# Optimization experiments

Measured on AMD Instinct MI355X. Metric: run time of the kernel, lower is better.

The kernel has to match this reference:

```python
import jax, jax.numpy as jnp
import numpy as np

KSIZE = 11
SIGMA = 1.5
CHANNELS = 1


def _gaussian_kernel(size=KSIZE, sigma=SIGMA, channels=CHANNELS):
    coords = jnp.arange(size, dtype=jnp.float32) - size // 2
    g = jnp.exp(-coords ** 2 / (2.0 * sigma ** 2))
    g = g / g.sum()
    k2d = jnp.outer(g, g)  # [k, k]
    # depthwise kernel, OIHW with I=1 per group
    return jnp.broadcast_to(k2d, (channels, 1, size, size))


def _dwconv(x, k):
    pad = KSIZE // 2
    return jax.lax.conv_general_dilated(
        x, k, window_strides=(1, 1), padding=[(pad, pad), (pad, pad)],
        dimension_numbers=('NCHW', 'OIHW', 'NCHW'),
        feature_group_count=CHANNELS)


def setup_inputs() -> dict:
    key = jax.random.key(0)
    k1, k2 = jax.random.split(key)
    x_hat = jax.random.normal(k1, (64, 1, 512, 512), dtype=jnp.float32)
    x = jax.random.normal(k2, (64, 1, 512, 512), dtype=jnp.float32)
    kernel = _gaussian_kernel()
    return {"x_hat": x_hat, "x": x, "kernel": kernel}


def reference(x_hat, x, kernel):
    C1, C2 = 0.01 ** 2, 0.03 ** 2
    # shift [-1,1] -> [0,1]
    a = (x + 1.0) / 2.0          # 'x' in _ssim
    b = (x_hat + 1.0) / 2.0      # 'y' in _ssim
    mu_x = _dwconv(a, kernel)
    mu_y = _dwconv(b, kernel)
    mu_x2 = mu_x ** 2
    mu_y2 = mu_y ** 2
    mu_xy = mu_x * mu_y
    sig_x = _dwconv(a * a, kernel) - mu_x2
    sig_y = _dwconv(b * b, kernel) - mu_y2
    sig_xy = _dwconv(a * b, kernel) - mu_xy
    num = (2.0 * mu_xy + C1) * (2.0 * sig_xy + C2)
    den = (mu_x2 + mu_y2 + C1) * (sig_x + sig_y + C2)
    ssim = (num / (den + 1e-08)).mean()
    return 1.0 - ssim
```

## Files before the change

### kernel.cpp

```cpp
#include <hip/hip_runtime.h>

#define IMG_W 512
#define IMG_H 512
#define RH    64
#define KS    11
#define KR    5
#define OFF   8
#define LROW  (OFF + IMG_W + OFF)

__global__ __launch_bounds__(256, 2)
void ssim_main(const float* __restrict__ xhat,
               const float* __restrict__ x,
               const float* __restrict__ kern,
               float* __restrict__ accum)
{
    __shared__ float rowA[LROW];
    __shared__ float rowB[LROW];
    __shared__ float red[4];

    const int tid   = threadIdx.x;
    const int c0    = tid << 1;
    const int img   = blockIdx.x >> 3;
    const int strip = blockIdx.x & 7;
    const int R0    = strip * RH;
    const float* xp = x    + (size_t)img * (IMG_W * IMG_H);
    const float* hp = xhat + (size_t)img * (IMG_W * IMG_H);

    float g[KS];
    {
        const float inv = rsqrtf(kern[5 * KS + 5]);
        #pragma unroll
        for (int i = 0; i < KS; ++i) g[i] = kern[5 * KS + i] * inv;
    }

    if (tid < OFF) {
        rowA[tid] = 0.f;                rowB[tid] = 0.f;
        rowA[OFF + IMG_W + tid] = 0.f;  rowB[OFF + IMG_W + tid] = 0.f;
    }

    float hist[5][KS][2];
    float acc = 0.f;
    const float C1 = 1e-4f, C2 = 9e-4f;

    #pragma unroll 1
    for (int rblk = 0; rblk < 77; rblk += 11) {
        #pragma unroll
        for (int p = 0; p < KS; ++p) {
            const int rr = rblk + p;
            const bool active = (rr < RH + 2 * KR);

            __syncthreads();
            if (active) {
                const int ri = R0 - KR + rr;
                float a0 = 0.f, a1 = 0.f, b0 = 0.f, b1 = 0.f;
                if (ri >= 0 && ri < IMG_H) {
                    const float2 vx = *(const float2*)(xp + (size_t)ri * IMG_W + c0);
                    const float2 vh = *(const float2*)(hp + (size_t)ri * IMG_W + c0);
                    a0 = fmaf(vx.x, 0.5f, 0.5f);
                    a1 = fmaf(vx.y, 0.5f, 0.5f);
                    b0 = fmaf(vh.x, 0.5f, 0.5f);
                    b1 = fmaf(vh.y, 0.5f, 0.5f);
                }
                *(float2*)&rowA[OFF + c0] = make_float2(a0, a1);
                *(float2*)&rowB[OFF + c0] = make_float2(b0, b1);
            }
            __syncthreads();

            if (active) {
                float h[5][2];
                #pragma unroll
                for (int f = 0; f < 5; ++f) { h[f][0] = 0.f; h[f][1] = 0.f; }
                const int ibase = OFF + c0 - KR;
                #pragma unroll
                for (int i = 0; i < KS + 1; ++i) {
                    const float pa  = rowA[ibase + i];
                    const float pb  = rowB[ibase + i];
                    const float paa = pa * pa;
                    const float pbb = pb * pb;
                    const float pab = pa * pb;
                    if (i < KS) {
                        const float w = g[i];
                        h[0][0] = fmaf(w, pa,  h[0][0]);
                        h[1][0] = fmaf(w, pb,  h[1][0]);
                        h[2][0] = fmaf(w, paa, h[2][0]);
                        h[3][0] = fmaf(w, pbb, h[3][0]);
                        h[4][0] = fmaf(w, pab, h[4][0]);
                    }
                    if (i > 0) {
                        const float w = g[i - 1];
                        h[0][1] = fmaf(w, pa,  h[0][1]);
                        h[1][1] = fmaf(w, pb,  h[1][1]);
                        h[2][1] = fmaf(w, paa, h[2][1]);
                        h[3][1] = fmaf(w, pbb, h[3][1]);
                        h[4][1] = fmaf(w, pab, h[4][1]);
                    }
                }
                #pragma unroll
                for (int f = 0; f < 5; ++f) {
                    hist[f][p][0] = h[f][0];
                    hist[f][p][1] = h[f][1];
                }

                if (rr >= 2 * KR) {
                    float v[5][2];
                    #pragma unroll
                    for (int f = 0; f < 5; ++f) { v[f][0] = 0.f; v[f][1] = 0.f; }
                    #pragma unroll
                    for (int t = 0; t < KS; ++t) {
                        const int slot = (p + 1 + t) % KS;
                        const float w = g[t];
                        #pragma unroll
                        for (int f = 0; f < 5; ++f) {
                            v[f][0] = fmaf(w, hist[f][slot][0], v[f][0]);
                            v[f][1] = fmaf(w, hist[f][slot][1], v[f][1]);
                        }
                    }
                    #pragma unroll
                    for (int col = 0; col < 2; ++col) {
                        const float mux  = v[0][col], muy = v[1][col];
                        const float mux2 = mux * mux;
                        const float muy2 = muy * muy;
                        const float muxy = mux * muy;
                        const float sx   = v[2][col] - mux2;
                        const float sy   = v[3][col] - muy2;
                        const float sxy  = v[4][col] - muxy;
                        const float num  = (2.f * muxy + C1) * (2.f * sxy + C2);
                        const float den  = (mux2 + muy2 + C1) * (sx + sy + C2);
                        acc += num / (den + 1e-8f);
                    }
                }
            }
        }
    }

    #pragma unroll
    for (int o = 32; o > 0; o >>= 1) acc += __shfl_down(acc, o, 64);
    if ((tid & 63) == 0) red[tid >> 6] = acc;
    __syncthreads();
    if (tid == 0) atomicAdd(accum, red[0] + red[1] + red[2] + red[3]);
}

__global__ void ssim_final(const float* __restrict__ accum,
                           float* __restrict__ out)
{
    out[0] = 1.0f - accum[0] * (1.0f / (64.0f * 512.0f * 512.0f));
}

extern "C" void kernel_launch(void* const* d_in, const int* in_sizes, int n_in,
                              void* d_out, int out_size, void* d_ws, size_t ws_size,
                              hipStream_t stream) {
    const float* xhat = (const float*)d_in[0];
    const float* xin  = (const float*)d_in[1];
    const float* kern = (const float*)d_in[2];
    float* out = (float*)d_out;
    float* ws  = (float*)d_ws;

    const int nimg   = in_sizes[0] / (IMG_W * IMG_H);
    const int strips = IMG_H / RH;
    const int nblk   = nimg * strips;

    hipMemsetAsync(ws, 0, sizeof(float), stream);
    ssim_main<<<nblk, 256, 0, stream>>>(xhat, xin, kern, ws);
    ssim_final<<<1, 1, 0, stream>>>(ws, out);
}
```

Baseline: 223.2 us.

## Split work into single-wave 128-column bands with halos and packed FMA

Replaces 256-thread blocks that each own a full-width 64-row strip with 64-thread, single-wavefront blocks that each own a 128-column by 32-row tile, loading left and right halo columns. The aim is more blocks for better occupancy and load balance, with __syncthreads becoming cheap within one wave. It also packs the A/B and AA/BB products into 2-wide vectors so the compiler can emit packed FMAs. The cost is more redundant halo rows and columns per tile (42 rows loaded for 32 output rows), extra scalar halo loads, and many more atomics.

```diff
diff --git a/kernel.cpp b/kernel.cpp
--- a/kernel.cpp
+++ b/kernel.cpp
@@ -1,14 +1,17 @@
 #include <hip/hip_runtime.h>
+
+typedef float v2f __attribute__((ext_vector_type(2)));
 
 #define IMG_W 512
 #define IMG_H 512
-#define RH    64
+#define RH    32
+#define BW    128
 #define KS    11
 #define KR    5
 #define OFF   8
-#define LROW  (OFF + IMG_W + OFF)
+#define LROW  (OFF + BW + OFF)
 
-__global__ __launch_bounds__(256, 2)
+__global__ __launch_bounds__(64, 4)
 void ssim_main(const float* __restrict__ xhat,
                const float* __restrict__ x,
                const float* __restrict__ kern,
@@ -16,12 +19,12 @@
 {
     __shared__ float rowA[LROW];
     __shared__ float rowB[LROW];
-    __shared__ float red[4];
 
-    const int tid   = threadIdx.x;
-    const int c0    = tid << 1;
-    const int img   = blockIdx.x >> 3;
-    const int strip = blockIdx.x & 7;
+    const int lane  = threadIdx.x;
+    const int band  = blockIdx.x & 3;
+    const int strip = (blockIdx.x >> 2) & 15;
+    const int img   = blockIdx.x >> 6;
+    const int base  = band * BW;
     const int R0    = strip * RH;
     const float* xp = x    + (size_t)img * (IMG_W * IMG_H);
     const float* hp = xhat + (size_t)img * (IMG_W * IMG_H);
@@ -33,111 +36,123 @@
         for (int i = 0; i < KS; ++i) g[i] = kern[5 * KS + i] * inv;
     }
 
-    if (tid < OFF) {
-        rowA[tid] = 0.f;                rowB[tid] = 0.f;
-        rowA[OFF + IMG_W + tid] = 0.f;  rowB[OFF + IMG_W + tid] = 0.f;
-    }
+    const int c0 = lane << 1;
+    const bool lhalo = lane < KR;
+    const bool rhalo = lane >= 64 - KR;
+    const int  lcol  = base - KR + lane;
+    const int  rcol  = base + BW + lane - (64 - KR);
 
-    float hist[5][KS][2];
+    v2f   hist01[KS][2];
+    v2f   hist23[KS][2];
+    float hist4 [KS][2];
     float acc = 0.f;
     const float C1 = 1e-4f, C2 = 9e-4f;
 
     #pragma unroll 1
-    for (int rblk = 0; rblk < 77; rblk += 11) {
-        #pragma unroll
-        for (int p = 0; p < KS; ++p) {
-            const int rr = rblk + p;
-            const bool active = (rr < RH + 2 * KR);
+    for (int rblk = 0; rblk < 44; rblk += 11) {
+      #pragma unroll
+      for (int p = 0; p < KS; ++p) {
+        const int rr = rblk + p;
+        const bool active = rr < RH + 2 * KR;
 
-            __syncthreads();
-            if (active) {
-                const int ri = R0 - KR + rr;
-                float a0 = 0.f, a1 = 0.f, b0 = 0.f, b1 = 0.f;
-                if (ri >= 0 && ri < IMG_H) {
-                    const float2 vx = *(const float2*)(xp + (size_t)ri * IMG_W + c0);
-                    const float2 vh = *(const float2*)(hp + (size_t)ri * IMG_W + c0);
-                    a0 = fmaf(vx.x, 0.5f, 0.5f);
-                    a1 = fmaf(vx.y, 0.5f, 0.5f);
-                    b0 = fmaf(vh.x, 0.5f, 0.5f);
-                    b1 = fmaf(vh.y, 0.5f, 0.5f);
+        __syncthreads();
+        if (active) {
+            const int ri  = R0 - KR + rr;
+            const bool rok = (ri >= 0) && (ri < IMG_H);
+            v2f av = {0.f, 0.f}, bv = {0.f, 0.f};
+            float la = 0.f, lb = 0.f, ra = 0.f, rb = 0.f;
+            if (rok) {
+                const size_t roff = (size_t)ri * IMG_W;
+                const float2 vx = *(const float2*)(xp + roff + base + c0);
+                const float2 vh = *(const float2*)(hp + roff + base + c0);
+                av.x = fmaf(vx.x, 0.5f, 0.5f); av.y = fmaf(vx.y, 0.5f, 0.5f);
+                bv.x = fmaf(vh.x, 0.5f, 0.5f); bv.y = fmaf(vh.y, 0.5f, 0.5f);
+                if (lhalo && lcol >= 0) {
+                    la = fmaf(xp[roff + lcol], 0.5f, 0.5f);
+                    lb = fmaf(hp[roff + lcol], 0.5f, 0.5f);
                 }
-                *(float2*)&rowA[OFF + c0] = make_float2(a0, a1);
-                *(float2*)&rowB[OFF + c0] = make_float2(b0, b1);
+                if (rhalo && rcol < IMG_W) {
+                    ra = fmaf(xp[roff + rcol], 0.5f, 0.5f);
+                    rb = fmaf(hp[roff + rcol], 0.5f, 0.5f);
+                }
             }
-            __syncthreads();
+            *(float2*)&rowA[OFF + c0] = make_float2(av.x, av.y);
+            *(float2*)&rowB[OFF + c0] = make_float2(bv.x, bv.y);
+            if (lhalo) { rowA[OFF - KR + lane] = la;
+                         rowB[OFF - KR + lane] = lb; }
+            if (rhalo) { rowA[OFF + BW + lane - (64 - KR)] = ra;
+                         rowB[OFF + BW + lane - (64 - KR)] = rb; }
+        }
+        __syncthreads();
 
-            if (active) {
-                float h[5][2];
+        if (active) {
+            v2f h01[2] = {{0.f,0.f},{0.f,0.f}};
+            v2f h23[2] = {{0.f,0.f},{0.f,0.f}};
+            float h4[2] = {0.f, 0.f};
+            const int ibase = OFF + c0 - KR;
+            #pragma unroll
+            for (int k = 0; k < KS + 1; ++k) {
+                v2f ab;
+                ab.x = rowA[ibase + k];
+                ab.y = rowB[ibase + k];
+                v2f  ab2 = ab * ab;
+                float pab = ab.x * ab.y;
+                if (k < KS) {
+                    const v2f w = {g[k], g[k]};
+                    h01[0] = __builtin_elementwise_fma(ab,  w, h01[0]);
+                    h23[0] = __builtin_elementwise_fma(ab2, w, h23[0]);
+                    h4[0]  = fmaf(pab, g[k], h4[0]);
+                }
+                if (k > 0) {
+                    const v2f w = {g[k-1], g[k-1]};
+                    h01[1] = __builtin_elementwise_fma(ab,  w, h01[1]);
+                    h23[1] = __builtin_elementwise_fma(ab2, w, h23[1]);
+                    h4[1]  = fmaf(pab, g[k-1], h4[1]);
+                }
+            }
+            #pragma unroll
+            for (int c = 0; c < 2; ++c) {
+                hist01[p][c] = h01[c];
+                hist23[p][c] = h23[c];
+                hist4 [p][c] = h4[c];
+            }
+
+            if (rr >= 2 * KR) {
+                v2f v01[2] = {{0.f,0.f},{0.f,0.f}};
+                v2f v23[2] = {{0.f,0.f},{0.f,0.f}};
+                float v4[2] = {0.f, 0.f};
                 #pragma unroll
-                for (int f = 0; f < 5; ++f) { h[f][0] = 0.f; h[f][1] = 0.f; }
-                const int ibase = OFF + c0 - KR;
-                #pragma unroll
-                for (int i = 0; i < KS + 1; ++i) {
-                    const float pa  = rowA[ibase + i];
-                    const float pb  = rowB[ibase + i];
-                    const float paa = pa * pa;
-                    const float pbb = pb * pb;
-                    const float pab = pa * pb;
-                    if (i < KS) {
-                        const float w = g[i];
-                        h[0][0] = fmaf(w, pa,  h[0][0]);
-                        h[1][0] = fmaf(w, pb,  h[1][0]);
-                        h[2][0] = fmaf(w, paa, h[2][0]);
-                        h[3][0] = fmaf(w, pbb, h[3][0]);
-                        h[4][0] = fmaf(w, pab, h[4][0]);
-                    }
-                    if (i > 0) {
-                        const float w = g[i - 1];
-                        h[0][1] = fmaf(w, pa,  h[0][1]);
-                        h[1][1] = fmaf(w, pb,  h[1][1]);
-                        h[2][1] = fmaf(w, paa, h[2][1]);
-                        h[3][1] = fmaf(w, pbb, h[3][1]);
-                        h[4][1] = fmaf(w, pab, h[4][1]);
+                for (int t = 0; t < KS; ++t) {
+                    const int slot = (p + 1 + t) % KS;
+                    const v2f w = {g[t], g[t]};
+                    #pragma unroll
+                    for (int c = 0; c < 2; ++c) {
+                        v01[c] = __builtin_elementwise_fma(hist01[slot][c], w, v01[c]);
+                        v23[c] = __builtin_elementwise_fma(hist23[slot][c], w, v23[c]);
+                        v4[c]  = fmaf(hist4[slot][c], g[t], v4[c]);
                     }
                 }
                 #pragma unroll
-                for (int f = 0; f < 5; ++f) {
-                    hist[f][p][0] = h[f][0];
-                    hist[f][p][1] = h[f][1];
-                }
-
-                if (rr >= 2 * KR) {
-                    float v[5][2];
-                    #pragma unroll
-                    for (int f = 0; f < 5; ++f) { v[f][0] = 0.f; v[f][1] = 0.f; }
-                    #pragma unroll
-                    for (int t = 0; t < KS; ++t) {
-                        const int slot = (p + 1 + t) % KS;
-                        const float w = g[t];
-                        #pragma unroll
-                        for (int f = 0; f < 5; ++f) {
-                            v[f][0] = fmaf(w, hist[f][slot][0], v[f][0]);
-                            v[f][1] = fmaf(w, hist[f][slot][1], v[f][1]);
-                        }
-                    }
-                    #pragma unroll
-                    for (int col = 0; col < 2; ++col) {
-                        const float mux  = v[0][col], muy = v[1][col];
-                        const float mux2 = mux * mux;
-                        const float muy2 = muy * muy;
-                        const float muxy = mux * muy;
-                        const float sx   = v[2][col] - mux2;
-                        const float sy   = v[3][col] - muy2;
-                        const float sxy  = v[4][col] - muxy;
-                        const float num  = (2.f * muxy + C1) * (2.f * sxy + C2);
-                        const float den  = (mux2 + muy2 + C1) * (sx + sy + C2);
-                        acc += num / (den + 1e-8f);
-                    }
+                for (int c = 0; c < 2; ++c) {
+                    const float mux  = v01[c].x, muy = v01[c].y;
+                    const float mux2 = mux * mux;
+                    const float muy2 = muy * muy;
+                    const float muxy = mux * muy;
+                    const float sx   = v23[c].x - mux2;
+                    const float sy   = v23[c].y - muy2;
+                    const float sxy  = v4[c]    - muxy;
+                    const float num  = (2.f * muxy + C1) * (2.f * sxy + C2);
+                    const float den  = (mux2 + muy2 + C1) * (sx + sy + C2);
+                    acc += num / (den + 1e-8f);
                 }
             }
         }
+      }
     }
 
     #pragma unroll
     for (int o = 32; o > 0; o >>= 1) acc += __shfl_down(acc, o, 64);
-    if ((tid & 63) == 0) red[tid >> 6] = acc;
-    __syncthreads();
-    if (tid == 0) atomicAdd(accum, red[0] + red[1] + red[2] + red[3]);
+    if (lane == 0) atomicAdd(accum, acc);
 }
 
 __global__ void ssim_final(const float* __restrict__ accum,
@@ -156,10 +171,9 @@
     float* ws  = (float*)d_ws;
 
     const int nimg   = in_sizes[0] / (IMG_W * IMG_H);
-    const int strips = IMG_H / RH;
-    const int nblk   = nimg * strips;
+    const int nblk   = nimg * (IMG_H / RH) * (IMG_W / BW);
 
     hipMemsetAsync(ws, 0, sizeof(float), stream);
-    ssim_main<<<nblk, 256, 0, stream>>>(xhat, xin, kern, ws);
+    ssim_main<<<nblk, 64, 0, stream>>>(xhat, xin, kern, ws);
     ssim_final<<<1, 1, 0, stream>>>(ws, out);
 }
```

New measurement: 506.3 us. 2.27x slower.
